# Kernel tuning notes

Measured on AMD Instinct MI355X. Metric: run time of the kernel, lower is better.

## Reference

```python
import jax, jax.numpy as jnp
import numpy as np

D_MODEL, H, D_FF = 1024, 16, 4096
B, S = 2, 2048
EPS = 1e-05


def layer_norm(x, gamma, beta):
    # Matches torch: mean and UNBIASED std over last dim, scalar gamma/beta,
    # and eps added to std (not variance).
    mean = jnp.mean(x, axis=-1, keepdims=True)
    var = jnp.sum((x - mean) ** 2, axis=-1, keepdims=True) / (x.shape[-1] - 1)
    return gamma * (x - mean) / (jnp.sqrt(var) + EPS) + beta


def setup_inputs() -> dict:
    key = jax.random.key(0)
    ks = jax.random.split(key, 16)
    sd = 1.0 / np.sqrt(D_MODEL)
    sf = 1.0 / np.sqrt(D_FF)
    return {
        "x": jax.random.normal(ks[0], (B, S, D_MODEL), jnp.float32),
        "mask": jnp.ones((1, 1, S, S), jnp.int32),
        "wq": jax.random.uniform(ks[1], (D_MODEL, D_MODEL), jnp.float32, -sd, sd),
        "bq": jax.random.uniform(ks[2], (D_MODEL,), jnp.float32, -sd, sd),
        "wk": jax.random.uniform(ks[3], (D_MODEL, D_MODEL), jnp.float32, -sd, sd),
        "bk": jax.random.uniform(ks[4], (D_MODEL,), jnp.float32, -sd, sd),
        "wv": jax.random.uniform(ks[5], (D_MODEL, D_MODEL), jnp.float32, -sd, sd),
        "bv": jax.random.uniform(ks[6], (D_MODEL,), jnp.float32, -sd, sd),
        "wo": jax.random.uniform(ks[7], (D_MODEL, D_MODEL), jnp.float32, -sd, sd),
        "bo": jax.random.uniform(ks[8], (D_MODEL,), jnp.float32, -sd, sd),
        "w1": jax.random.uniform(ks[9], (D_FF, D_MODEL), jnp.float32, -sd, sd),
        "b1": jax.random.uniform(ks[10], (D_FF,), jnp.float32, -sd, sd),
        "w2": jax.random.uniform(ks[11], (D_MODEL, D_FF), jnp.float32, -sf, sf),
        "b2": jax.random.uniform(ks[12], (D_MODEL,), jnp.float32, -sf, sf),
        "gamma1": jnp.ones((1,), jnp.float32),
        "beta1": jnp.zeros((1,), jnp.float32),
        "gamma2": jnp.ones((1,), jnp.float32),
        "beta2": jnp.zeros((1,), jnp.float32),
    }


def reference(x, mask, wq, bq, wk, bk, wv, bv, wo, bo, w1, b1, w2, b2,
              gamma1, beta1, gamma2, beta2):
    d_k = D_MODEL // H

    # --- residual 1: pre-LN self-attention ---
    xn = layer_norm(x, gamma1, beta1)
    q = (xn @ wq.T + bq).reshape(B, S, H, d_k).transpose(0, 2, 1, 3)
    k = (xn @ wk.T + bk).reshape(B, S, H, d_k).transpose(0, 2, 1, 3)
    v = (xn @ wv.T + bv).reshape(B, S, H, d_k).transpose(0, 2, 1, 3)

    scores = jnp.einsum("bhqd,bhkd->bhqk", q, k) / jnp.sqrt(
        jnp.asarray(d_k, x.dtype))
    scores = jnp.where(mask == 0, jnp.asarray(-1e9, x.dtype), scores)
    attn = jax.nn.softmax(scores, axis=-1)
    ctx = jnp.einsum("bhqk,bhkd->bhqd", attn, v)
    ctx = ctx.transpose(0, 2, 1, 3).reshape(B, S, D_MODEL)
    x = x + (ctx @ wo.T + bo)

    # --- residual 2: pre-LN feed-forward ---
    xn = layer_norm(x, gamma2, beta2)
    h = jax.nn.relu(xn @ w1.T + b1)
    x = x + (h @ w2.T + b2)
    return x
```

## Files before the change

kernel.cpp:

```cpp
#include <hip/hip_runtime.h>


typedef __bf16 bf16_t;
typedef __attribute__((ext_vector_type(8))) __bf16 bf16x8;
typedef __attribute__((ext_vector_type(4))) __bf16 bf16x4;
typedef __attribute__((ext_vector_type(2))) __bf16 bf16x2;
typedef __attribute__((ext_vector_type(4))) float f32x4;
typedef __attribute__((ext_vector_type(16))) float f32x16;
typedef __attribute__((ext_vector_type(2))) unsigned uint32x2;
typedef __attribute__((ext_vector_type(4))) unsigned uint32x4;

#define MB (1024ull * 1024ull)
#define QSCALE 0.18033688011112043f

__device__ __forceinline__ void gload_lds16(const bf16_t* g, bf16_t* l) {
    __builtin_amdgcn_global_load_lds(
        (const __attribute__((address_space(1))) void*)g,
        (__attribute__((address_space(3))) void*)l, 16, 0, 0);
}

__device__ __forceinline__ int bswz(int row) { return ((row >> 1) & 3) << 3; }

__device__ __forceinline__ int swz(int row, int col) {
    return row * 64 + ((((col >> 3) ^ row) & 7) << 3) + (col & 7);
}

__device__ __forceinline__ unsigned cvtpk(float a, float b) {
    bf16x2 v = {(__bf16)a, (__bf16)b};
    return __builtin_bit_cast(unsigned, v);
}

__global__ __launch_bounds__(256) void cvt_all(
    const float* __restrict__ wq, const float* __restrict__ wk,
    const float* __restrict__ wv, const float* __restrict__ wo,
    const float* __restrict__ w1, const float* __restrict__ w2,
    bf16_t* __restrict__ wqkv, bf16_t* __restrict__ wob, bf16_t* __restrict__ w1b,
    bf16_t* __restrict__ w2b) {
    const int b = blockIdx.x, t = threadIdx.x;
    const float* in;
    bf16_t* out;
    int i;
    if (b < 1024) { in = wq; out = wqkv; i = b * 256 + t; }
    else if (b < 2048) { in = wk; out = wqkv + 1048576; i = (b - 1024) * 256 + t; }
    else if (b < 3072) { in = wv; out = wqkv + 2097152; i = (b - 2048) * 256 + t; }
    else if (b < 4096) { in = wo; out = wob; i = (b - 3072) * 256 + t; }
    else if (b < 8192) { in = w1; out = w1b; i = (b - 4096) * 256 + t; }
    else { in = w2; out = w2b; i = (b - 8192) * 256 + t; }
    float4 v = ((const float4*)in)[i];
    bf16x4 o = {(__bf16)v.x, (__bf16)v.y, (__bf16)v.z, (__bf16)v.w};
    ((bf16x4*)out)[i] = o;
}

__global__ __launch_bounds__(256) void ln_kernel(const float* __restrict__ x,
                                                 bf16_t* __restrict__ out,
                                                 const float* __restrict__ gamma,
                                                 const float* __restrict__ beta) {
    const int lane = threadIdx.x & 63;
    const int row = blockIdx.x * 4 + (threadIdx.x >> 6);
    const float* xr = x + (size_t)row * 1024;
    float4 v[4];
    float s = 0.f;
#pragma unroll
    for (int i = 0; i < 4; ++i) {
        v[i] = ((const float4*)xr)[i * 64 + lane];
        s += v[i].x + v[i].y + v[i].z + v[i].w;
    }
#pragma unroll
    for (int o = 32; o; o >>= 1) s += __shfl_xor(s, o);
    float mean = s * (1.f / 1024.f);
    float vs = 0.f;
#pragma unroll
    for (int i = 0; i < 4; ++i) {
        float a = v[i].x - mean, b = v[i].y - mean, c = v[i].z - mean, d = v[i].w - mean;
        vs += a * a + b * b + c * c + d * d;
    }
#pragma unroll
    for (int o = 32; o; o >>= 1) vs += __shfl_xor(vs, o);
    float inv = 1.f / (sqrtf(vs * (1.f / 1023.f)) + 1e-5f);
    float g = gamma[0] * inv, bb = beta[0];
    bf16_t* orow = out + (size_t)row * 1024;
#pragma unroll
    for (int i = 0; i < 4; ++i) {
        bf16x4 ov = {(__bf16)((v[i].x - mean) * g + bb), (__bf16)((v[i].y - mean) * g + bb),
                     (__bf16)((v[i].z - mean) * g + bb), (__bf16)((v[i].w - mean) * g + bb)};
        *(bf16x4*)(orow + (i * 64 + lane) * 4) = ov;
    }
}

template <int KERN>
__global__ __launch_bounds__(512, 2) void gemm256(
    const bf16_t* __restrict__ A, const bf16_t* __restrict__ Bw, int K,
    const float* __restrict__ bias0, const float* __restrict__ bias1,
    const float* __restrict__ bias2, void* __restrict__ o0, void* __restrict__ o1,
    void* __restrict__ o2) {
    __shared__ bf16_t L[4 * 16384];
    const int t = threadIdx.x, lane = t & 63, w = t >> 6;
    const int wm = w >> 2, wn = w & 3;
    const int l15 = lane & 15, l4 = lane >> 4;
    const int bm = blockIdx.x, bn = blockIdx.y;
    const int NT = K >> 5;
    const bf16_t* Ab = A + (size_t)bm * 256 * K;
    const bf16_t* Bb = Bw + (size_t)bn * 256 * K;
    const int srow = t >> 2, pcol = (t & 3) * 8;
    f32x4 acc[8][4] = {};

    auto stageA = [&](int tt) {
        bf16_t* s = L + (tt & 3) * 16384;
        const int kb = tt * 32;
#pragma unroll
        for (int i = 0; i < 2; ++i) {
            int row = i * 128 + srow;
            int lcol = pcol ^ bswz(row);
            gload_lds16(Ab + (size_t)row * K + kb + lcol, s + i * 4096 + t * 8);
        }
    };
    auto stageB = [&](int tt) {
        bf16_t* s = L + (tt & 3) * 16384 + 8192;
        const int kb = tt * 32;
#pragma unroll
        for (int i = 0; i < 2; ++i) {
            int row = i * 128 + srow;
            int lcol = pcol ^ bswz(row);
            gload_lds16(Bb + (size_t)row * K + kb + lcol, s + i * 4096 + t * 8);
        }
    };

    stageA(0); stageB(0); stageA(1); stageB(1); stageA(2); stageB(2);
    asm volatile("s_waitcnt vmcnt(8)" ::: "memory");
    __builtin_amdgcn_s_barrier();

    for (int tt = 0; tt < NT; ++tt) {
        bf16_t* s = L + (tt & 3) * 16384;
        bf16_t* sB = s + 8192;
        bf16x8 af[4], bfr[4];
#pragma unroll
        for (int m = 0; m < 4; ++m) {
            int row = wm * 128 + m * 16 + l15;
            af[m] = *(const bf16x8*)(s + row * 32 + ((l4 * 8) ^ bswz(row)));
        }
#pragma unroll
        for (int n = 0; n < 4; ++n) {
            int row = wn * 64 + n * 16 + l15;
            bfr[n] = *(const bf16x8*)(sB + row * 32 + ((l4 * 8) ^ bswz(row)));
        }
        if (tt + 3 < NT) stageA(tt + 3);
        __builtin_amdgcn_s_barrier();
        __builtin_amdgcn_s_setprio(1);
#pragma unroll
        for (int m = 0; m < 4; ++m)
#pragma unroll
            for (int n = 0; n < 4; ++n)
                acc[m][n] = __builtin_amdgcn_mfma_f32_16x16x32_bf16(af[m], bfr[n], acc[m][n],
                                                                   0, 0, 0);
        __builtin_amdgcn_s_setprio(0);
        __builtin_amdgcn_s_barrier();
#pragma unroll
        for (int m = 0; m < 4; ++m) {
            int row = wm * 128 + 64 + m * 16 + l15;
            af[m] = *(const bf16x8*)(s + row * 32 + ((l4 * 8) ^ bswz(row)));
        }
        if (tt + 3 < NT) stageB(tt + 3);
        __builtin_amdgcn_s_barrier();
        __builtin_amdgcn_s_setprio(1);
#pragma unroll
        for (int m = 0; m < 4; ++m)
#pragma unroll
            for (int n = 0; n < 4; ++n)
                acc[4 + m][n] = __builtin_amdgcn_mfma_f32_16x16x32_bf16(af[m], bfr[n],
                                                                       acc[4 + m][n], 0, 0, 0);
        __builtin_amdgcn_s_setprio(0);
        if (tt + 3 < NT)
            asm volatile("s_waitcnt vmcnt(8)" ::: "memory");
        else if (tt + 2 < NT)
            asm volatile("s_waitcnt vmcnt(4)" ::: "memory");
        else
            asm volatile("s_waitcnt vmcnt(0)" ::: "memory");
        __builtin_amdgcn_s_barrier();
    }

    if (KERN == 1) {
        const int colb = bn * 256 + wn * 64;
        float bb[4];
#pragma unroll
        for (int n = 0; n < 4; ++n) bb[n] = bias0[colb + n * 16 + l15];
#pragma unroll
        for (int m = 0; m < 8; ++m) {
            const int row0 = bm * 256 + wm * 128 + m * 16 + (l4 << 2);
#pragma unroll
            for (int n = 0; n < 4; ++n)
#pragma unroll
                for (int j = 0; j < 4; ++j) {
                    float v = acc[m][n][j] + bb[n];
                    ((bf16_t*)o0)[(size_t)(row0 + j) * 4096 + colb + n * 16 + l15] =
                        (bf16_t)(v > 0.f ? v : 0.f);
                }
        }
        return;
    }
    if (bn < 8) {
        const bool isq = bn < 4;
        const float* bias = isq ? bias0 : bias1;
        const int head = (bn & 3) * 4 + wn;
        const int b = (bm * 256) >> 11;
        const int srow0 = (bm * 256 + wm * 128) & 2047;
        bf16_t* dst = (bf16_t*)(isq ? o0 : o1) + ((size_t)(b * 16 + head) << 17);
        float bb[4];
#pragma unroll
        for (int n = 0; n < 4; ++n) bb[n] = bias[head * 64 + n * 16 + l15];
#pragma unroll
        for (int m = 0; m < 8; ++m)
#pragma unroll
            for (int n = 0; n < 4; ++n)
#pragma unroll
                for (int j = 0; j < 4; ++j) {
                    int srw = srow0 + m * 16 + (l4 << 2) + j;
                    float v = acc[m][n][j] + bb[n];
                    if (isq) v *= QSCALE;
                    dst[((size_t)srw << 6) + n * 16 + l15] = (bf16_t)v;
                }
    } else {
        const int head = (bn - 8) * 4 + wn;
        const int b = (bm * 256) >> 11;
        const int sbase = (bm * 256 + wm * 128) & 2047;
        bf16_t* P = L + w * 8192;
        float bb[4];
#pragma unroll
        for (int n = 0; n < 4; ++n) bb[n] = bias2[head * 64 + n * 16 + l15];
#pragma unroll
        for (int m = 0; m < 8; ++m)
#pragma unroll
            for (int n = 0; n < 4; ++n) {
                int d = n * 16 + l15;
                int sl = m * 16 + (l4 << 2);
                bf16x4 pk = {(__bf16)(acc[m][n][0] + bb[n]), (__bf16)(acc[m][n][1] + bb[n]),
                             (__bf16)(acc[m][n][2] + bb[n]), (__bf16)(acc[m][n][3] + bb[n])};
                *(bf16x4*)(P + d * 128 + (sl ^ ((d & 7) << 3))) = pk;
            }
#pragma unroll
        for (int p = 0; p < 16; ++p) {
            int id = p * 64 + lane;
            int d = id >> 4, c8 = (id & 15) * 8;
            bf16x8 vv = *(const bf16x8*)(P + d * 128 + (c8 ^ ((d & 7) << 3)));
            *(bf16x8*)((bf16_t*)o2 + (((size_t)(b * 16 + head) * 64 + d) << 11) + sbase + c8) =
                vv;
        }
    }
}

template <int SPLIT>
__global__ __launch_bounds__(256, 2) void gemm128sq(
    const bf16_t* __restrict__ A, const bf16_t* __restrict__ Bw, int stride, int Ks,
    const float* __restrict__ bias, const float* __restrict__ resid,
    void* __restrict__ o0, void* __restrict__ o1) {
    __shared__ bf16_t L[4 * 8192];
    const int t = threadIdx.x, lane = t & 63, w = t >> 6;
    const int wr = w >> 1, wc = w & 1;
    const int l15 = lane & 15, l4 = lane >> 4;
    const int bm = blockIdx.x, bn = blockIdx.y;
    const int NT = Ks >> 5;
    const size_t kofs = SPLIT ? (size_t)blockIdx.z * Ks : 0;
    const bf16_t* Ab = A + (size_t)bm * 128 * stride + kofs;
    const bf16_t* Bb = Bw + (size_t)bn * 128 * stride + kofs;
    const int srow = t >> 2, pcol = (t & 3) * 8;
    f32x4 acc[4][4] = {};

    auto STAGE = [&](int tt) {
        bf16_t* s = L + (tt & 3) * 8192;
        const int kb = tt * 32;
#pragma unroll
        for (int i = 0; i < 2; ++i) {
            int row = i * 64 + srow;
            int lcol = pcol ^ bswz(row);
            gload_lds16(Ab + (size_t)row * stride + kb + lcol, s + i * 2048 + t * 8);
            gload_lds16(Bb + (size_t)row * stride + kb + lcol, s + 4096 + i * 2048 + t * 8);
        }
    };

    STAGE(0); STAGE(1); STAGE(2);
    asm volatile("s_waitcnt vmcnt(8)" ::: "memory");
    __builtin_amdgcn_s_barrier();

    for (int tt = 0; tt < NT; ++tt) {
        bf16_t* s = L + (tt & 3) * 8192;
        bf16x8 af[4], bfr[4];
#pragma unroll
        for (int m = 0; m < 4; ++m) {
            int row = wr * 64 + m * 16 + l15;
            af[m] = *(const bf16x8*)(s + row * 32 + ((l4 * 8) ^ bswz(row)));
        }
#pragma unroll
        for (int n = 0; n < 4; ++n) {
            int row = wc * 64 + n * 16 + l15;
            bfr[n] = *(const bf16x8*)(s + 4096 + row * 32 + ((l4 * 8) ^ bswz(row)));
        }
        if (tt + 3 < NT) STAGE(tt + 3);
        __builtin_amdgcn_s_barrier();
        __builtin_amdgcn_s_setprio(1);
#pragma unroll
        for (int m = 0; m < 4; ++m)
#pragma unroll
            for (int n = 0; n < 4; ++n)
                acc[m][n] = __builtin_amdgcn_mfma_f32_16x16x32_bf16(af[m], bfr[n], acc[m][n],
                                                                   0, 0, 0);
        __builtin_amdgcn_s_setprio(0);
        if (tt + 3 < NT)
            asm volatile("s_waitcnt vmcnt(8)" ::: "memory");
        else if (tt + 2 < NT)
            asm volatile("s_waitcnt vmcnt(4)" ::: "memory");
        else
            asm volatile("s_waitcnt vmcnt(0)" ::: "memory");
        __builtin_amdgcn_s_barrier();
    }

#pragma unroll
    for (int m = 0; m < 4; ++m) {
        const int row0 = bm * 128 + wr * 64 + m * 16 + (l4 << 2);
#pragma unroll
        for (int n = 0; n < 4; ++n) {
            const int col = bn * 128 + wc * 64 + n * 16 + l15;
#pragma unroll
            for (int j = 0; j < 4; ++j) {
                const int row = row0 + j;
                if (SPLIT == 0) {
                    ((float*)o0)[(size_t)row * 1024 + col] =
                        resid[(size_t)row * 1024 + col] + acc[m][n][j] + bias[col];
                } else {
                    bf16_t* po = (bf16_t*)(blockIdx.z ? o1 : o0);
                    po[(size_t)row * 1024 + col] = (bf16_t)acc[m][n][j];
                }
            }
        }
    }
}

__global__ __launch_bounds__(256) void ffn2_combine(
    const bf16_t* __restrict__ p0, const bf16_t* __restrict__ p1,
    const float* __restrict__ resid, const float* __restrict__ bias,
    float* __restrict__ out) {
    int i = blockIdx.x * 256 + threadIdx.x;
    float4 r = ((const float4*)resid)[i];
    bf16x4 a = ((const bf16x4*)p0)[i];
    bf16x4 b = ((const bf16x4*)p1)[i];
    float4 bs = ((const float4*)bias)[i & 255];
    float4 o;
    o.x = r.x + (float)a.x + (float)b.x + bs.x;
    o.y = r.y + (float)a.y + (float)b.y + bs.y;
    o.z = r.z + (float)a.z + (float)b.z + bs.z;
    o.w = r.w + (float)a.w + (float)b.w + bs.w;
    ((float4*)out)[i] = o;
}

__global__ __launch_bounds__(256, 2) void attn_kernel(const bf16_t* __restrict__ q,
                                                      const bf16_t* __restrict__ k,
                                                      const bf16_t* __restrict__ vt,
                                                      bf16_t* __restrict__ ctx) {
    __shared__ bf16_t Kl[64 * 64];
    __shared__ bf16_t Vl[64 * 64];
    const int t = threadIdx.x, lane = t & 63, w = t >> 6;
    const int bid = blockIdx.x;
    const int xcd = bid & 7, j = bid >> 3;
    const int bh = xcd + ((j >> 4) << 3);
    const int qx = j & 15;
    const bf16_t* qg = q + (size_t)bh * 2048 * 64;
    const bf16_t* kg = k + (size_t)bh * 2048 * 64;
    const bf16_t* vg = vt + (size_t)bh * 64 * 2048;
    const int r = t >> 3, c8 = (t & 7) * 8;
    const int l31 = lane & 31, h = lane >> 5;
    const int qrow = qx * 128 + w * 32 + l31;

    bf16x8 qf[4];
#pragma unroll
    for (int kd = 0; kd < 4; ++kd)
        qf[kd] = *(const bf16x8*)(qg + (size_t)qrow * 64 + kd * 16 + h * 8);

    f32x16 o0 = {}, o1 = {};
    float mi = -1e30f, li = 0.f;

    {
        bf16x8 k0 = *(const bf16x8*)(kg + (size_t)r * 64 + c8);
        bf16x8 k1 = *(const bf16x8*)(kg + (size_t)(r + 32) * 64 + c8);
        bf16x8 v0 = *(const bf16x8*)(vg + (size_t)r * 2048 + c8);
        bf16x8 v1 = *(const bf16x8*)(vg + (size_t)(r + 32) * 2048 + c8);
        *(bf16x8*)(Kl + swz(r, c8)) = k0;
        *(bf16x8*)(Kl + swz(r + 32, c8)) = k1;
        *(bf16x8*)(Vl + swz(r, c8)) = v0;
        *(bf16x8*)(Vl + swz(r + 32, c8)) = v1;
    }

    for (int kt = 0; kt < 2048; kt += 64) {
        __syncthreads();
        bf16x8 k0, k1, v0, v1;
        const bool more = (kt + 64) < 2048;
        if (more) {
            k0 = *(const bf16x8*)(kg + (size_t)(kt + 64 + r) * 64 + c8);
            k1 = *(const bf16x8*)(kg + (size_t)(kt + 64 + r + 32) * 64 + c8);
            v0 = *(const bf16x8*)(vg + (size_t)r * 2048 + kt + 64 + c8);
            v1 = *(const bf16x8*)(vg + (size_t)(r + 32) * 2048 + kt + 64 + c8);
        }
        f32x16 sT0 = {}, sT1 = {};
        __builtin_amdgcn_s_setprio(1);
#pragma unroll
        for (int kd = 0; kd < 4; ++kd) {
            bf16x8 ka0 = *(const bf16x8*)(Kl + swz(l31, kd * 16 + h * 8));
            bf16x8 ka1 = *(const bf16x8*)(Kl + swz(32 + l31, kd * 16 + h * 8));
            sT0 = __builtin_amdgcn_mfma_f32_32x32x16_bf16(ka0, qf[kd], sT0, 0, 0, 0);
            sT1 = __builtin_amdgcn_mfma_f32_32x32x16_bf16(ka1, qf[kd], sT1, 0, 0, 0);
        }
        __builtin_amdgcn_s_setprio(0);
        float mx = fmaxf(sT0[0], sT0[1]);
#pragma unroll
        for (int i = 2; i < 16; ++i) mx = fmaxf(mx, sT0[i]);
#pragma unroll
        for (int i = 0; i < 16; ++i) mx = fmaxf(mx, sT1[i]);
        mx = fmaxf(mx, __shfl_xor(mx, 32));
        if (!__all(mx <= mi + 8.f)) {
            float mn = fmaxf(mi, mx);
            float al = __builtin_amdgcn_exp2f(mi - mn);
            mi = mn;
            li *= al;
            o0 *= al;
            o1 *= al;
        }
        f32x16 e0, e1;
        float rs = 0.f;
#pragma unroll
        for (int i = 0; i < 16; ++i) {
            e0[i] = __builtin_amdgcn_exp2f(sT0[i] - mi);
            rs += e0[i];
        }
#pragma unroll
        for (int i = 0; i < 16; ++i) {
            e1[i] = __builtin_amdgcn_exp2f(sT1[i] - mi);
            rs += e1[i];
        }
        rs += __shfl_xor(rs, 32);
        li += rs;
        bf16x8 pa[4];
#pragma unroll
        for (int kd = 0; kd < 4; ++kd) {
            const f32x16& e = (kd < 2) ? e0 : e1;
            const int R0l = 8 * (kd & 1);
            const int R0h = R0l + 4;
            unsigned U0 = cvtpk(e[R0l + 0], e[R0l + 1]);
            unsigned V0 = cvtpk(e[R0l + 2], e[R0l + 3]);
            unsigned U1 = cvtpk(e[R0h + 0], e[R0h + 1]);
            unsigned V1 = cvtpk(e[R0h + 2], e[R0h + 3]);
            uint32x2 ru = __builtin_amdgcn_permlane32_swap(U0, U1, false, false);
            uint32x2 rv = __builtin_amdgcn_permlane32_swap(V0, V1, false, false);
            uint32x4 pw = {ru.x, rv.x, ru.y, rv.y};
            pa[kd] = __builtin_bit_cast(bf16x8, pw);
        }
        __builtin_amdgcn_s_setprio(1);
#pragma unroll
        for (int kd = 0; kd < 4; ++kd) {
            bf16x8 va0 = *(const bf16x8*)(Vl + swz(l31, kd * 16 + h * 8));
            bf16x8 va1 = *(const bf16x8*)(Vl + swz(32 + l31, kd * 16 + h * 8));
            o0 = __builtin_amdgcn_mfma_f32_32x32x16_bf16(va0, pa[kd], o0, 0, 0, 0);
            o1 = __builtin_amdgcn_mfma_f32_32x32x16_bf16(va1, pa[kd], o1, 0, 0, 0);
        }
        __builtin_amdgcn_s_setprio(0);
        __syncthreads();
        if (more) {
            *(bf16x8*)(Kl + swz(r, c8)) = k0;
            *(bf16x8*)(Kl + swz(r + 32, c8)) = k1;
            *(bf16x8*)(Vl + swz(r, c8)) = v0;
            *(bf16x8*)(Vl + swz(r + 32, c8)) = v1;
        }
    }
    float inv = 1.f / li;
    size_t base = ((size_t)(bh >> 4) * 2048 + qrow) * 1024 + (bh & 15) * 64;
#pragma unroll
    for (int g = 0; g < 4; ++g) {
        bf16x4 ov0 = {(__bf16)(o0[4 * g + 0] * inv), (__bf16)(o0[4 * g + 1] * inv),
                      (__bf16)(o0[4 * g + 2] * inv), (__bf16)(o0[4 * g + 3] * inv)};
        *(bf16x4*)(ctx + base + 8 * g + 4 * h) = ov0;
        bf16x4 ov1 = {(__bf16)(o1[4 * g + 0] * inv), (__bf16)(o1[4 * g + 1] * inv),
                      (__bf16)(o1[4 * g + 2] * inv), (__bf16)(o1[4 * g + 3] * inv)};
        *(bf16x4*)(ctx + base + 32 + 8 * g + 4 * h) = ov1;
    }
}

extern "C" void kernel_launch(void* const* d_in, const int* in_sizes, int n_in,
                              void* d_out, int out_size, void* d_ws, size_t ws_size,
                              hipStream_t stream) {
    const float* x = (const float*)d_in[0];
    const float* wq = (const float*)d_in[2];
    const float* bq = (const float*)d_in[3];
    const float* wk = (const float*)d_in[4];
    const float* bk = (const float*)d_in[5];
    const float* wv = (const float*)d_in[6];
    const float* bv = (const float*)d_in[7];
    const float* wo = (const float*)d_in[8];
    const float* bo = (const float*)d_in[9];
    const float* w1 = (const float*)d_in[10];
    const float* b1 = (const float*)d_in[11];
    const float* w2 = (const float*)d_in[12];
    const float* b2 = (const float*)d_in[13];
    const float* gamma1 = (const float*)d_in[14];
    const float* beta1 = (const float*)d_in[15];
    const float* gamma2 = (const float*)d_in[16];
    const float* beta2 = (const float*)d_in[17];

    char* ws = (char*)d_ws;
    bf16_t* wqkv = (bf16_t*)(ws + 0);
    bf16_t* wob = (bf16_t*)(ws + 6 * MB);
    bf16_t* w1b = (bf16_t*)(ws + 8 * MB);
    bf16_t* w2b = (bf16_t*)(ws + 16 * MB);
    bf16_t* xnb = (bf16_t*)(ws + 24 * MB);
    bf16_t* qb = (bf16_t*)(ws + 32 * MB);
    bf16_t* kb = (bf16_t*)(ws + 40 * MB);
    bf16_t* vtb = (bf16_t*)(ws + 48 * MB);
    bf16_t* ctxb = (bf16_t*)(ws + 56 * MB);
    float* x1 = (float*)(ws + 64 * MB);
    bf16_t* hb = (bf16_t*)(ws + 32 * MB);
    bf16_t* p0 = (bf16_t*)(ws + 0);
    bf16_t* p1 = (bf16_t*)(ws + 24 * MB);

    cvt_all<<<12288, 256, 0, stream>>>(wq, wk, wv, wo, w1, w2, wqkv, wob, w1b, w2b);

    ln_kernel<<<1024, 256, 0, stream>>>(x, xnb, gamma1, beta1);
    gemm256<0><<<dim3(16, 12), 512, 0, stream>>>(xnb, wqkv, 1024, bq, bk, bv, qb, kb, vtb);
    attn_kernel<<<512, 256, 0, stream>>>(qb, kb, vtb, ctxb);
    gemm128sq<0><<<dim3(32, 8), 256, 0, stream>>>(ctxb, wob, 1024, 1024, bo, x, x1, nullptr);
    ln_kernel<<<1024, 256, 0, stream>>>(x1, xnb, gamma2, beta2);
    gemm256<1><<<dim3(16, 16), 512, 0, stream>>>(xnb, w1b, 1024, b1, nullptr, nullptr, hb,
                                                 nullptr, nullptr);
    gemm128sq<1><<<dim3(32, 8, 2), 256, 0, stream>>>(hb, w2b, 4096, 2048, nullptr, nullptr,
                                                     p0, p1);
    ffn2_combine<<<4096, 256, 0, stream>>>(p0, p1, x1, b2, (float*)d_out);
}
```

Measured before the change: 212.4 us.

## Split attention KV sequence across two wave groups and merge partial softmax

The attention kernel now runs 512 threads per block. Two halves of four waves each process separate halves of the key/value sequence using their own LDS buffers, which halves the serial loop length per wave. The second half writes its running max, sum and partial outputs (as bf16) to shared memory, and the first half merges them flash-decoding style before storing. This raises in-flight waves and parallelism, at the cost of more LDS, an extra merge step and bf16 rounding of the partial outputs.

After: 224.0 us. 5.5% more time.

```diff
diff --git a/kernel.cpp b/kernel.cpp
--- a/kernel.cpp
+++ b/kernel.cpp
@@ -350,13 +350,16 @@
     ((float4*)out)[i] = o;
 }
 
-__global__ __launch_bounds__(256, 2) void attn_kernel(const bf16_t* __restrict__ q,
+__global__ __launch_bounds__(512, 2) void attn_kernel(const bf16_t* __restrict__ q,
                                                       const bf16_t* __restrict__ k,
                                                       const bf16_t* __restrict__ vt,
                                                       bf16_t* __restrict__ ctx) {
-    __shared__ bf16_t Kl[64 * 64];
-    __shared__ bf16_t Vl[64 * 64];
+    __shared__ bf16_t Kl[2][64 * 64];
+    __shared__ bf16_t Vl[2][64 * 64];
+    __shared__ float Ml[4][64][2];
+    __shared__ bf16_t Ol[4][64][32];
     const int t = threadIdx.x, lane = t & 63, w = t >> 6;
+    const int half = w >> 2, wq = w & 3;
     const int bid = blockIdx.x;
     const int xcd = bid & 7, j = bid >> 3;
     const int bh = xcd + ((j >> 4) << 3);
@@ -364,9 +367,11 @@
     const bf16_t* qg = q + (size_t)bh * 2048 * 64;
     const bf16_t* kg = k + (size_t)bh * 2048 * 64;
     const bf16_t* vg = vt + (size_t)bh * 64 * 2048;
-    const int r = t >> 3, c8 = (t & 7) * 8;
+    const int hb = t >> 8, ts = t & 255;
+    const int r = ts >> 3, c8 = (ts & 7) * 8;
+    const int sbase = hb << 10;
     const int l31 = lane & 31, h = lane >> 5;
-    const int qrow = qx * 128 + w * 32 + l31;
+    const int qrow = qx * 128 + wq * 32 + l31;
 
     bf16x8 qf[4];
 #pragma unroll
@@ -377,32 +382,34 @@
     float mi = -1e30f, li = 0.f;
 
     {
-        bf16x8 k0 = *(const bf16x8*)(kg + (size_t)r * 64 + c8);
-        bf16x8 k1 = *(const bf16x8*)(kg + (size_t)(r + 32) * 64 + c8);
-        bf16x8 v0 = *(const bf16x8*)(vg + (size_t)r * 2048 + c8);
-        bf16x8 v1 = *(const bf16x8*)(vg + (size_t)(r + 32) * 2048 + c8);
-        *(bf16x8*)(Kl + swz(r, c8)) = k0;
-        *(bf16x8*)(Kl + swz(r + 32, c8)) = k1;
-        *(bf16x8*)(Vl + swz(r, c8)) = v0;
-        *(bf16x8*)(Vl + swz(r + 32, c8)) = v1;
-    }
-
-    for (int kt = 0; kt < 2048; kt += 64) {
+        bf16x8 k0 = *(const bf16x8*)(kg + (size_t)(sbase + r) * 64 + c8);
+        bf16x8 k1 = *(const bf16x8*)(kg + (size_t)(sbase + r + 32) * 64 + c8);
+        bf16x8 v0 = *(const bf16x8*)(vg + (size_t)r * 2048 + sbase + c8);
+        bf16x8 v1 = *(const bf16x8*)(vg + (size_t)(r + 32) * 2048 + sbase + c8);
+        *(bf16x8*)(Kl[hb] + swz(r, c8)) = k0;
+        *(bf16x8*)(Kl[hb] + swz(r + 32, c8)) = k1;
+        *(bf16x8*)(Vl[hb] + swz(r, c8)) = v0;
+        *(bf16x8*)(Vl[hb] + swz(r + 32, c8)) = v1;
+    }
+
+    for (int kt = 0; kt < 1024; kt += 64) {
         __syncthreads();
         bf16x8 k0, k1, v0, v1;
-        const bool more = (kt + 64) < 2048;
+        const bool more = (kt + 64) < 1024;
         if (more) {
-            k0 = *(const bf16x8*)(kg + (size_t)(kt + 64 + r) * 64 + c8);
-            k1 = *(const bf16x8*)(kg + (size_t)(kt + 64 + r + 32) * 64 + c8);
-            v0 = *(const bf16x8*)(vg + (size_t)r * 2048 + kt + 64 + c8);
-            v1 = *(const bf16x8*)(vg + (size_t)(r + 32) * 2048 + kt + 64 + c8);
-        }
+            k0 = *(const bf16x8*)(kg + (size_t)(sbase + kt + 64 + r) * 64 + c8);
+            k1 = *(const bf16x8*)(kg + (size_t)(sbase + kt + 64 + r + 32) * 64 + c8);
+            v0 = *(const bf16x8*)(vg + (size_t)r * 2048 + sbase + kt + 64 + c8);
+            v1 = *(const bf16x8*)(vg + (size_t)(r + 32) * 2048 + sbase + kt + 64 + c8);
+        }
+        const bf16_t* Kb = Kl[half];
+        const bf16_t* Vb = Vl[half];
         f32x16 sT0 = {}, sT1 = {};
         __builtin_amdgcn_s_setprio(1);
 #pragma unroll
         for (int kd = 0; kd < 4; ++kd) {
-            bf16x8 ka0 = *(const bf16x8*)(Kl + swz(l31, kd * 16 + h * 8));
-            bf16x8 ka1 = *(const bf16x8*)(Kl + swz(32 + l31, kd * 16 + h * 8));
+            bf16x8 ka0 = *(const bf16x8*)(Kb + swz(l31, kd * 16 + h * 8));
+            bf16x8 ka1 = *(const bf16x8*)(Kb + swz(32 + l31, kd * 16 + h * 8));
             sT0 = __builtin_amdgcn_mfma_f32_32x32x16_bf16(ka0, qf[kd], sT0, 0, 0, 0);
             sT1 = __builtin_amdgcn_mfma_f32_32x32x16_bf16(ka1, qf[kd], sT1, 0, 0, 0);
         }
@@ -453,30 +460,51 @@
         __builtin_amdgcn_s_setprio(1);
 #pragma unroll
         for (int kd = 0; kd < 4; ++kd) {
-            bf16x8 va0 = *(const bf16x8*)(Vl + swz(l31, kd * 16 + h * 8));
-            bf16x8 va1 = *(const bf16x8*)(Vl + swz(32 + l31, kd * 16 + h * 8));
+            bf16x8 va0 = *(const bf16x8*)(Vb + swz(l31, kd * 16 + h * 8));
+            bf16x8 va1 = *(const bf16x8*)(Vb + swz(32 + l31, kd * 16 + h * 8));
             o0 = __builtin_amdgcn_mfma_f32_32x32x16_bf16(va0, pa[kd], o0, 0, 0, 0);
             o1 = __builtin_amdgcn_mfma_f32_32x32x16_bf16(va1, pa[kd], o1, 0, 0, 0);
         }
         __builtin_amdgcn_s_setprio(0);
         __syncthreads();
         if (more) {
-            *(bf16x8*)(Kl + swz(r, c8)) = k0;
-            *(bf16x8*)(Kl + swz(r + 32, c8)) = k1;
-            *(bf16x8*)(Vl + swz(r, c8)) = v0;
-            *(bf16x8*)(Vl + swz(r + 32, c8)) = v1;
-        }
-    }
-    float inv = 1.f / li;
-    size_t base = ((size_t)(bh >> 4) * 2048 + qrow) * 1024 + (bh & 15) * 64;
-#pragma unroll
-    for (int g = 0; g < 4; ++g) {
-        bf16x4 ov0 = {(__bf16)(o0[4 * g + 0] * inv), (__bf16)(o0[4 * g + 1] * inv),
-                      (__bf16)(o0[4 * g + 2] * inv), (__bf16)(o0[4 * g + 3] * inv)};
-        *(bf16x4*)(ctx + base + 8 * g + 4 * h) = ov0;
-        bf16x4 ov1 = {(__bf16)(o1[4 * g + 0] * inv), (__bf16)(o1[4 * g + 1] * inv),
-                      (__bf16)(o1[4 * g + 2] * inv), (__bf16)(o1[4 * g + 3] * inv)};
-        *(bf16x4*)(ctx + base + 32 + 8 * g + 4 * h) = ov1;
+            *(bf16x8*)(Kl[hb] + swz(r, c8)) = k0;
+            *(bf16x8*)(Kl[hb] + swz(r + 32, c8)) = k1;
+            *(bf16x8*)(Vl[hb] + swz(r, c8)) = v0;
+            *(bf16x8*)(Vl[hb] + swz(r + 32, c8)) = v1;
+        }
+    }
+
+    if (half == 1) {
+        Ml[wq][lane][0] = mi;
+        Ml[wq][lane][1] = li;
+#pragma unroll
+        for (int i = 0; i < 16; ++i) {
+            Ol[wq][lane][i] = (bf16_t)o0[i];
+            Ol[wq][lane][16 + i] = (bf16_t)o1[i];
+        }
+    }
+    __syncthreads();
+    if (half == 0) {
+        float mb = Ml[wq][lane][0], lb = Ml[wq][lane][1];
+        float m = fmaxf(mi, mb);
+        float a = __builtin_amdgcn_exp2f(mi - m);
+        float bsc = __builtin_amdgcn_exp2f(mb - m);
+        float inv = 1.f / (li * a + lb * bsc);
+        float ia = a * inv, ib = bsc * inv;
+        size_t base = ((size_t)(bh >> 4) * 2048 + qrow) * 1024 + (bh & 15) * 64;
+#pragma unroll
+        for (int g = 0; g < 4; ++g) {
+            bf16x4 ov0, ov1;
+#pragma unroll
+            for (int jj = 0; jj < 4; ++jj) {
+                int i = 4 * g + jj;
+                ov0[jj] = (__bf16)(o0[i] * ia + (float)Ol[wq][lane][i] * ib);
+                ov1[jj] = (__bf16)(o1[i] * ia + (float)Ol[wq][lane][16 + i] * ib);
+            }
+            *(bf16x4*)(ctx + base + 8 * g + 4 * h) = ov0;
+            *(bf16x4*)(ctx + base + 32 + 8 * g + 4 * h) = ov1;
+        }
     }
 }
 
@@ -520,7 +548,7 @@
 
     ln_kernel<<<1024, 256, 0, stream>>>(x, xnb, gamma1, beta1);
     gemm256<0><<<dim3(16, 12), 512, 0, stream>>>(xnb, wqkv, 1024, bq, bk, bv, qb, kb, vtb);
-    attn_kernel<<<512, 256, 0, stream>>>(qb, kb, vtb, ctxb);
+    attn_kernel<<<512, 512, 0, stream>>>(qb, kb, vtb, ctxb);
     gemm128sq<0><<<dim3(32, 8), 256, 0, stream>>>(ctxb, wob, 1024, 1024, bo, x, x1, nullptr);
     ln_kernel<<<1024, 256, 0, stream>>>(x1, xnb, gamma2, beta2);
     gemm256<1><<<dim3(16, 16), 512, 0, stream>>>(xnb, w1b, 1024, b1, nullptr, nullptr, hb,
```

## Split attention over key halves and merge partial softmax results

Applied to the files above, without the earlier changes.

The attention kernel now splits each (batch, head, query-tile) job along the key dimension into two halves. This doubles the block count to 1024, and each block writes unnormalized partial outputs plus per-row max and sum values. A new merge kernel rescales the two partials with exp2 of the max differences and writes the normalized context in the original layout. The aim is more parallelism and latency hiding per CU, at the cost of an extra launch, about 16MB of extra partial traffic, and bf16 rounding of the unnormalized partials.

Result: slower. 221.3 us (+4.2%).

```diff
diff --git a/kernel.cpp b/kernel.cpp
--- a/kernel.cpp
+++ b/kernel.cpp
@@ -350,23 +350,27 @@
     ((float4*)out)[i] = o;
 }
 
-__global__ __launch_bounds__(256, 2) void attn_kernel(const bf16_t* __restrict__ q,
-                                                      const bf16_t* __restrict__ k,
-                                                      const bf16_t* __restrict__ vt,
-                                                      bf16_t* __restrict__ ctx) {
+__global__ __launch_bounds__(256, 2) void attn_split(const bf16_t* __restrict__ q,
+                                                     const bf16_t* __restrict__ k,
+                                                     const bf16_t* __restrict__ vt,
+                                                     bf16_t* __restrict__ opart,
+                                                     float2* __restrict__ ml) {
     __shared__ bf16_t Kl[64 * 64];
     __shared__ bf16_t Vl[64 * 64];
     const int t = threadIdx.x, lane = t & 63, w = t >> 6;
     const int bid = blockIdx.x;
     const int xcd = bid & 7, j = bid >> 3;
-    const int bh = xcd + ((j >> 4) << 3);
-    const int qx = j & 15;
+    const int bh = xcd + ((j >> 5) << 3);
+    const int qx = (j & 31) >> 1;
+    const int half = j & 1;
+    const int sbase = half << 10;
     const bf16_t* qg = q + (size_t)bh * 2048 * 64;
     const bf16_t* kg = k + (size_t)bh * 2048 * 64;
     const bf16_t* vg = vt + (size_t)bh * 64 * 2048;
     const int r = t >> 3, c8 = (t & 7) * 8;
     const int l31 = lane & 31, h = lane >> 5;
-    const int qrow = qx * 128 + w * 32 + l31;
+    const int rowl = w * 32 + l31;
+    const int qrow = qx * 128 + rowl;
 
     bf16x8 qf[4];
 #pragma unroll
@@ -377,25 +381,25 @@
     float mi = -1e30f, li = 0.f;
 
     {
-        bf16x8 k0 = *(const bf16x8*)(kg + (size_t)r * 64 + c8);
-        bf16x8 k1 = *(const bf16x8*)(kg + (size_t)(r + 32) * 64 + c8);
-        bf16x8 v0 = *(const bf16x8*)(vg + (size_t)r * 2048 + c8);
-        bf16x8 v1 = *(const bf16x8*)(vg + (size_t)(r + 32) * 2048 + c8);
+        bf16x8 k0 = *(const bf16x8*)(kg + (size_t)(sbase + r) * 64 + c8);
+        bf16x8 k1 = *(const bf16x8*)(kg + (size_t)(sbase + r + 32) * 64 + c8);
+        bf16x8 v0 = *(const bf16x8*)(vg + (size_t)r * 2048 + sbase + c8);
+        bf16x8 v1 = *(const bf16x8*)(vg + (size_t)(r + 32) * 2048 + sbase + c8);
         *(bf16x8*)(Kl + swz(r, c8)) = k0;
         *(bf16x8*)(Kl + swz(r + 32, c8)) = k1;
         *(bf16x8*)(Vl + swz(r, c8)) = v0;
         *(bf16x8*)(Vl + swz(r + 32, c8)) = v1;
     }
 
-    for (int kt = 0; kt < 2048; kt += 64) {
+    for (int kt = 0; kt < 1024; kt += 64) {
         __syncthreads();
         bf16x8 k0, k1, v0, v1;
-        const bool more = (kt + 64) < 2048;
+        const bool more = (kt + 64) < 1024;
         if (more) {
-            k0 = *(const bf16x8*)(kg + (size_t)(kt + 64 + r) * 64 + c8);
-            k1 = *(const bf16x8*)(kg + (size_t)(kt + 64 + r + 32) * 64 + c8);
-            v0 = *(const bf16x8*)(vg + (size_t)r * 2048 + kt + 64 + c8);
-            v1 = *(const bf16x8*)(vg + (size_t)(r + 32) * 2048 + kt + 64 + c8);
+            k0 = *(const bf16x8*)(kg + (size_t)(sbase + kt + 64 + r) * 64 + c8);
+            k1 = *(const bf16x8*)(kg + (size_t)(sbase + kt + 64 + r + 32) * 64 + c8);
+            v0 = *(const bf16x8*)(vg + (size_t)r * 2048 + sbase + kt + 64 + c8);
+            v1 = *(const bf16x8*)(vg + (size_t)(r + 32) * 2048 + sbase + kt + 64 + c8);
         }
         f32x16 sT0 = {}, sT1 = {};
         __builtin_amdgcn_s_setprio(1);
@@ -467,17 +471,41 @@
             *(bf16x8*)(Vl + swz(r + 32, c8)) = v1;
         }
     }
-    float inv = 1.f / li;
-    size_t base = ((size_t)(bh >> 4) * 2048 + qrow) * 1024 + (bh & 15) * 64;
+    const int combo = bh * 16 + qx;
+    bf16_t* op = opart + ((size_t)half << 22) + (size_t)combo * 8192 + (size_t)rowl * 64;
 #pragma unroll
     for (int g = 0; g < 4; ++g) {
-        bf16x4 ov0 = {(__bf16)(o0[4 * g + 0] * inv), (__bf16)(o0[4 * g + 1] * inv),
-                      (__bf16)(o0[4 * g + 2] * inv), (__bf16)(o0[4 * g + 3] * inv)};
-        *(bf16x4*)(ctx + base + 8 * g + 4 * h) = ov0;
-        bf16x4 ov1 = {(__bf16)(o1[4 * g + 0] * inv), (__bf16)(o1[4 * g + 1] * inv),
-                      (__bf16)(o1[4 * g + 2] * inv), (__bf16)(o1[4 * g + 3] * inv)};
-        *(bf16x4*)(ctx + base + 32 + 8 * g + 4 * h) = ov1;
-    }
+        bf16x4 ov0 = {(__bf16)o0[4 * g + 0], (__bf16)o0[4 * g + 1], (__bf16)o0[4 * g + 2],
+                      (__bf16)o0[4 * g + 3]};
+        *(bf16x4*)(op + 8 * g + 4 * h) = ov0;
+        bf16x4 ov1 = {(__bf16)o1[4 * g + 0], (__bf16)o1[4 * g + 1], (__bf16)o1[4 * g + 2],
+                      (__bf16)o1[4 * g + 3]};
+        *(bf16x4*)(op + 32 + 8 * g + 4 * h) = ov1;
+    }
+    if (h == 0) ml[((size_t)half * 512 + combo) * 128 + rowl] = make_float2(mi, li);
+}
+
+__global__ __launch_bounds__(256) void attn_merge(const bf16_t* __restrict__ opart,
+                                                  const float2* __restrict__ ml,
+                                                  bf16_t* __restrict__ ctx) {
+    const int combo = blockIdx.x >> 2;
+    const int row = (blockIdx.x & 3) * 32 + (threadIdx.x >> 3);
+    const int d8 = (threadIdx.x & 7) * 8;
+    float2 a = ml[(size_t)combo * 128 + row];
+    float2 b = ml[(size_t)(512 + combo) * 128 + row];
+    float m = fmaxf(a.x, b.x);
+    float ea = __builtin_amdgcn_exp2f(a.x - m), eb = __builtin_amdgcn_exp2f(b.x - m);
+    float inv = 1.f / (a.y * ea + b.y * eb);
+    float ia = ea * inv, ib = eb * inv;
+    size_t po = (size_t)combo * 8192 + (size_t)row * 64 + d8;
+    bf16x8 u = *(const bf16x8*)(opart + po);
+    bf16x8 v = *(const bf16x8*)(opart + (1ull << 22) + po);
+    bf16x8 o;
+#pragma unroll
+    for (int jj = 0; jj < 8; ++jj) o[jj] = (__bf16)((float)u[jj] * ia + (float)v[jj] * ib);
+    const int bh = combo >> 4, qx = combo & 15;
+    const int rg = qx * 128 + row;
+    *(bf16x8*)(ctx + ((size_t)(bh >> 4) * 2048 + rg) * 1024 + (bh & 15) * 64 + d8) = o;
 }
 
 extern "C" void kernel_launch(void* const* d_in, const int* in_sizes, int n_in,
@@ -513,6 +541,8 @@
     bf16_t* ctxb = (bf16_t*)(ws + 56 * MB);
     float* x1 = (float*)(ws + 64 * MB);
     bf16_t* hb = (bf16_t*)(ws + 32 * MB);
+    bf16_t* opart = (bf16_t*)(ws + 64 * MB);
+    float2* mlbuf = (float2*)(ws + 0);
     bf16_t* p0 = (bf16_t*)(ws + 0);
     bf16_t* p1 = (bf16_t*)(ws + 24 * MB);
 
@@ -520,7 +550,8 @@
 
     ln_kernel<<<1024, 256, 0, stream>>>(x, xnb, gamma1, beta1);
     gemm256<0><<<dim3(16, 12), 512, 0, stream>>>(xnb, wqkv, 1024, bq, bk, bv, qb, kb, vtb);
-    attn_kernel<<<512, 256, 0, stream>>>(qb, kb, vtb, ctxb);
+    attn_split<<<1024, 256, 0, stream>>>(qb, kb, vtb, opart, mlbuf);
+    attn_merge<<<2048, 256, 0, stream>>>(opart, mlbuf, ctxb);
     gemm128sq<0><<<dim3(32, 8), 256, 0, stream>>>(ctxb, wob, 1024, 1024, bo, x, x1, nullptr);
     ln_kernel<<<1024, 256, 0, stream>>>(x1, xnb, gamma2, beta2);
     gemm256<1><<<dim3(16, 16), 512, 0, stream>>>(xnb, w1b, 1024, b1, nullptr, nullptr, hb,
```
